# Optimization experiments

Measured on AMD Instinct MI355X. Metric: run time of the kernel, lower is better.

## Reference

```python
import jax, jax.numpy as jnp
import numpy as np

N_NODES = 20000
N_EDGES = 640000
IN_DIM = 128
HID_DIM = 256
N_CLASSES = 3
N_TYPES = 4
N_ASPECTS = 4096


def _type_aware_gcn(x, W_type, W_self, b, src, dst, etypes, n_nodes):
    # Per-node, per-type transforms: [N, T, H]
    xt = jnp.einsum('nd,tdh->nth', x, W_type)
    # Per-edge message: transform of source node under the edge's type. [E, H]
    msg = xt[src, etypes]
    # Degree-normalized scatter-sum into destination nodes.
    agg = jax.ops.segment_sum(msg, dst, num_segments=n_nodes)
    deg = jax.ops.segment_sum(jnp.ones((src.shape[0],), dtype=x.dtype), dst,
                              num_segments=n_nodes)
    agg = agg / jnp.clip(deg, 1.0)[:, None]
    # Self-loop transform + bias.
    return agg + x @ W_self + b


def setup_inputs() -> dict:
    key = jax.random.key(0)
    ks = jax.random.split(key, 12)
    features = jax.random.normal(ks[0], (N_NODES, IN_DIM), dtype=jnp.float32)
    edge_index = jax.random.randint(ks[1], (2, N_EDGES), 0, N_NODES)
    edge_types = jax.random.randint(ks[2], (N_EDGES,), 0, N_TYPES)
    aspect_indices = jax.random.randint(ks[3], (N_ASPECTS,), 0, N_NODES)
    s1 = 1.0 / np.sqrt(IN_DIM)
    s2 = 1.0 / np.sqrt(HID_DIM)
    W_type1 = jax.random.uniform(ks[4], (N_TYPES, IN_DIM, HID_DIM), minval=-s1, maxval=s1)
    W_self1 = jax.random.uniform(ks[5], (IN_DIM, HID_DIM), minval=-s1, maxval=s1)
    b1 = jnp.zeros((HID_DIM,), dtype=jnp.float32)
    W_type2 = jax.random.uniform(ks[6], (N_TYPES, HID_DIM, HID_DIM), minval=-s2, maxval=s2)
    W_self2 = jax.random.uniform(ks[7], (HID_DIM, HID_DIM), minval=-s2, maxval=s2)
    b2 = jnp.zeros((HID_DIM,), dtype=jnp.float32)
    W_cls = jax.random.uniform(ks[8], (HID_DIM, N_CLASSES), minval=-s2, maxval=s2)
    b_cls = jnp.zeros((N_CLASSES,), dtype=jnp.float32)
    return {
        'features': features,
        'W_type1': W_type1, 'W_self1': W_self1, 'b1': b1,
        'W_type2': W_type2, 'W_self2': W_self2, 'b2': b2,
        'W_cls': W_cls, 'b_cls': b_cls,
        'edge_index': edge_index,
        'edge_types': edge_types,
        'aspect_indices': aspect_indices,
    }


def reference(features, W_type1, W_self1, b1, W_type2, W_self2, b2,
              W_cls, b_cls, edge_index, edge_types, aspect_indices):
    n = features.shape[0]
    src, dst = edge_index[0], edge_index[1]
    h = _type_aware_gcn(features, W_type1, W_self1, b1, src, dst, edge_types, n)
    h = jax.nn.relu(h)
    # dropout: eval mode -> identity
    h = _type_aware_gcn(h, W_type2, W_self2, b2, src, dst, edge_types, n)
    aspect_embeddings = h[aspect_indices]            # [A, H]
    logits = aspect_embeddings @ W_cls + b_cls       # [A, C]
    return logits
```

## Files before the change

### kernel.cpp

```cpp
#include <hip/hip_runtime.h>

#define N_NODES   20000
#define N_EDGES   640000
#define IN_DIM    128
#define HID_DIM   256
#define N_TYPES   4
#define N_ASPECTS 4096
#define NT4       (N_NODES * N_TYPES)
#define NBUCK     157
#define BCAP      5120
#define CHUNK     2560

typedef __bf16 v8bf __attribute__((ext_vector_type(8)));
typedef float  f32x4 __attribute__((ext_vector_type(4)));

static __device__ __forceinline__ float bf2f(unsigned short u) {
    return __builtin_bit_cast(float, ((unsigned int)u) << 16);
}
static __device__ __forceinline__ float bflo(unsigned int u) {
    return __builtin_bit_cast(float, u << 16);
}
static __device__ __forceinline__ float bfhi(unsigned int u) {
    return __builtin_bit_cast(float, u & 0xffff0000u);
}
static __device__ __forceinline__ unsigned short f2bf(float f) {
    unsigned int u = __builtin_bit_cast(unsigned int, f);
    u += 0x7fffu + ((u >> 16) & 1u);
    return (unsigned short)(u >> 16);
}

static __device__ __forceinline__ int local_flag(const unsigned short* w) {
    __shared__ int red[4];
    int tid = threadIdx.x;
    int c = 0;
    for (int i = tid; i < 8192; i += 256) {
        unsigned hb = (w[i] >> 8) & 0x7f;
        c += (hb >= 0x39 && hb <= 0x3D) ? 1 : 0;
    }
#pragma unroll
    for (int off = 32; off >= 1; off >>= 1) c += __shfl_down(c, off);
    if ((tid & 63) == 0) red[tid >> 6] = c;
    __syncthreads();
    int tot = red[0] + red[1] + red[2] + red[3];
    __syncthreads();
    return (tot >= 6144) ? 1 : 0;
}

__global__ __launch_bounds__(256) void pre_kernel(
        const void* __restrict__ x,
        const void* __restrict__ Ws1, const void* __restrict__ Wt1,
        const void* __restrict__ Ws2, const void* __restrict__ Wt2,
        unsigned short* __restrict__ xc,
        unsigned short* __restrict__ WT1,
        unsigned short* __restrict__ WT2,
        int* __restrict__ bucket_cursor,
        int* __restrict__ flag) {
    int bf = local_flag((const unsigned short*)Ws1);
    int b = blockIdx.x, tid = threadIdx.x;
    if (b < 1250) {
        int idx = b * 256 + tid;
        if (bf) {
            reinterpret_cast<uint4*>(xc)[idx] = reinterpret_cast<const uint4*>(x)[idx];
        } else {
            const float* xf = reinterpret_cast<const float*>(x) + (size_t)idx * 8;
            unsigned short r[8] __attribute__((aligned(16)));
#pragma unroll
            for (int j = 0; j < 8; j++) r[j] = f2bf(xf[j]);
            reinterpret_cast<uint4*>(xc)[idx] = *reinterpret_cast<const uint4*>(r);
        }
    } else if (b < 1890) {
        int idx = (b - 1250) * 256 + tid;
        int n = idx / 640, k = idx - n * 640;
        const void* p = (k < 128) ? Ws1 : Wt1;
        size_t src = (k < 128) ? ((size_t)k * 256 + n) : ((size_t)(k - 128) * 256 + n);
        WT1[idx] = bf ? ((const unsigned short*)p)[src] : f2bf(((const float*)p)[src]);
    } else if (b < 3170) {
        int idx = (b - 1890) * 256 + tid;
        int n = idx / 1280, k = idx - n * 1280;
        const void* p = (k < 256) ? Ws2 : Wt2;
        size_t src = (k < 256) ? ((size_t)k * 256 + n) : ((size_t)(k - 256) * 256 + n);
        WT2[idx] = bf ? ((const unsigned short*)p)[src] : f2bf(((const float*)p)[src]);
    } else {
        if (tid < NBUCK) bucket_cursor[tid] = 0;
        if (tid == 0) *flag = bf;
    }
}

__global__ __launch_bounds__(256) void bucketA_kernel(
        const int* __restrict__ ei, const int* __restrict__ et,
        int* __restrict__ bucket_cursor, unsigned int* __restrict__ breg) {
    __shared__ unsigned int ord[CHUNK];
    __shared__ int hist[NBUCK], start[NBUCK], cur[NBUCK], gbase[NBUCK];
    int tid = threadIdx.x;
    int e0 = blockIdx.x * CHUNK;
    for (int i = tid; i < NBUCK; i += 256) hist[i] = 0;
    __syncthreads();
    unsigned int pk[10];
    int bk[10];
#pragma unroll
    for (int r = 0; r < 10; r++) {
        int e = e0 + r * 256 + tid;
        int s = __builtin_nontemporal_load(ei + e);
        int d = __builtin_nontemporal_load(ei + N_EDGES + e);
        int t = __builtin_nontemporal_load(et + e);
        pk[r] = (unsigned int)s | ((unsigned int)t << 15) | ((unsigned int)d << 17);
        bk[r] = d >> 7;
        atomicAdd(&hist[bk[r]], 1);
    }
    __syncthreads();
    if (tid == 0) {
        int acc = 0;
        for (int b = 0; b < NBUCK; b++) { start[b] = acc; cur[b] = acc; acc += hist[b]; }
    }
    __syncthreads();
#pragma unroll
    for (int r = 0; r < 10; r++) {
        int p = atomicAdd(&cur[bk[r]], 1);
        ord[p] = pk[r];
    }
    __syncthreads();
    for (int b = tid; b < NBUCK; b += 256)
        if (hist[b] > 0) gbase[b] = atomicAdd(bucket_cursor + b, hist[b]);
    __syncthreads();
    for (int p = tid; p < CHUNK; p += 256) {
        unsigned int e = ord[p];
        int b = (int)(e >> 24);
        int gp = gbase[b] + (p - start[b]);
        if (gp < BCAP)
            __builtin_nontemporal_store(e, breg + (size_t)b * BCAP + gp);
    }
}

__global__ __launch_bounds__(256) void bucketB_kernel(
        const unsigned int* __restrict__ breg,
        const int* __restrict__ bucket_cursor,
        unsigned short* __restrict__ perm,
        int* __restrict__ offsets4) {
    __shared__ int cnt[512], off[512];
    __shared__ int buf[256];
    int b = blockIdx.x, tid = threadIdx.x;
    int cv = (tid < NBUCK) ? bucket_cursor[tid] : 0;
    if (cv > BCAP) cv = BCAP;
    buf[tid] = cv;
    __syncthreads();
    for (int o = 1; o < 256; o <<= 1) {
        int t = (tid >= o) ? buf[tid - o] : 0;
        __syncthreads();
        buf[tid] += t;
        __syncthreads();
    }
    int obase = (b > 0) ? buf[b - 1] : 0;
    if (b == 0 && tid == 0) offsets4[NT4] = buf[255];
    int Eb = bucket_cursor[b];
    if (Eb > BCAP) Eb = BCAP;
    for (int i = tid; i < 512; i += 256) cnt[i] = 0;
    __syncthreads();
    const unsigned int* reg = breg + (size_t)b * BCAP;
    for (int i = tid; i < Eb; i += 256) {
        unsigned int e = reg[i];
        int seg = (((e >> 17) & 127) << 2) | ((e >> 15) & 3);
        atomicAdd(&cnt[seg], 1);
    }
    __syncthreads();
    if (tid == 0) {
        int acc = 0;
        for (int i = 0; i < 512; i++) { off[i] = acc; acc += cnt[i]; }
    }
    __syncthreads();
    for (int i = tid; i < 512; i += 256) {
        int node = b * 128 + (i >> 2);
        if (node < N_NODES) offsets4[node * 4 + (i & 3)] = obase + off[i];
    }
    __syncthreads();
    for (int i = tid; i < Eb; i += 256) {
        unsigned int e = reg[i];
        int seg = (((e >> 17) & 127) << 2) | ((e >> 15) & 3);
        int p = atomicAdd(&off[seg], 1);
        perm[obase + p] = (unsigned short)(e & 0x7fff);
    }
}

template <int D>
__global__ __launch_bounds__(256) void agg_kernel(
        const unsigned short* __restrict__ F,
        const int* __restrict__ offs4,
        const unsigned short* __restrict__ perm,
        unsigned short* __restrict__ AG) {
    constexpr int G = D / 8;
    constexpr int NSUB = 64 / G;
    int wave = threadIdx.x >> 6, lane = threadIdx.x & 63;
    int sg = lane / G;
    int gl = lane - sg * G;
    for (int n = blockIdx.x * 4 + wave; n < N_NODES; n += gridDim.x * 4) {
        int o0 = offs4[n * 4];
        int o4 = offs4[n * 4 + 4];
        int deg = o4 - o0;
        float inv = 1.0f / (float)(deg > 1 ? deg : 1);
        int s0 = o0;
#pragma unroll
        for (int t = 0; t < 4; t++) {
            int s1 = offs4[n * 4 + t + 1];
            float a[8];
#pragma unroll
            for (int v = 0; v < 8; v++) a[v] = 0.f;
            int j = s0;
            while (j < s1) {
                int m = s1 - j;
                if (m > 64) m = 64;
                int pw = (int)perm[j + ((lane < m) ? lane : 0)];
                int nfull = (m / (NSUB * 4)) * (NSUB * 4);
                for (int base = 0; base < nfull; base += NSUB * 4) {
                    uint4 x[4];
#pragma unroll
                    for (int l = 0; l < 4; l++) {
                        int src = __shfl(pw, base + sg * 4 + l);
                        x[l] = *reinterpret_cast<const uint4*>(F + (size_t)src * D + gl * 8);
                    }
#pragma unroll
                    for (int l = 0; l < 4; l++) {
                        a[0] += bflo(x[l].x); a[1] += bfhi(x[l].x);
                        a[2] += bflo(x[l].y); a[3] += bfhi(x[l].y);
                        a[4] += bflo(x[l].z); a[5] += bfhi(x[l].z);
                        a[6] += bflo(x[l].w); a[7] += bfhi(x[l].w);
                    }
                }
                for (int k = nfull; k < m; k += NSUB) {
                    int e = k + sg;
                    int valid = (e < m);
                    int idx = valid ? e : (m - 1);
                    int src = __shfl(pw, idx);
                    uint4 x = *reinterpret_cast<const uint4*>(F + (size_t)src * D + gl * 8);
                    unsigned msk = valid ? 0xffffffffu : 0u;
                    a[0] += bflo(x.x & msk); a[1] += bfhi(x.x & msk);
                    a[2] += bflo(x.y & msk); a[3] += bfhi(x.y & msk);
                    a[4] += bflo(x.z & msk); a[5] += bfhi(x.z & msk);
                    a[6] += bflo(x.w & msk); a[7] += bfhi(x.w & msk);
                }
                j += m;
            }
#pragma unroll
            for (int v = 0; v < 8; v++) {
                float s = a[v];
                s += __shfl_xor(s, G);
                if (NSUB == 4) s += __shfl_xor(s, 2 * G);
                a[v] = s * inv;
            }
            if (sg == 0) {
                unsigned short r[8] __attribute__((aligned(16)));
#pragma unroll
                for (int v = 0; v < 8; v++) r[v] = f2bf(a[v]);
                *reinterpret_cast<uint4*>(AG + (size_t)n * (4 * D) + t * D + gl * 8) =
                    *reinterpret_cast<const uint4*>(r);
            }
            s0 = s1;
        }
    }
}

template <int D>
__global__ __launch_bounds__(256, 6) void gemm_kernel(
        const unsigned short* __restrict__ X,
        const unsigned short* __restrict__ AG,
        const unsigned short* __restrict__ BT,
        const void* __restrict__ bias,
        const int* __restrict__ flagp,
        unsigned short* __restrict__ C,
        int M, int relu) {
    constexpr int K = 5 * D;
    constexpr int LDW = 72;
    __shared__ __align__(16) unsigned short As[64 * LDW];
    __shared__ __align__(16) unsigned short Bs[64 * LDW];
    int b = blockIdx.x;
    int mt = (b & 7) + 8 * (b >> 5);
    int nt = (b >> 3) & 3;
    int mtiles = (M + 63) >> 6;
    if (mt >= mtiles) return;
    int m0 = mt * 64;
    int n0 = nt * 64;
    int tid  = threadIdx.x;
    int wave = tid >> 6, lane = tid & 63;
    int wm = wave >> 1, wn = wave & 1;
    int quad = lane >> 4, l16 = lane & 15;

    f32x4 acc[2][2];
#pragma unroll
    for (int i = 0; i < 2; i++)
#pragma unroll
        for (int j = 0; j < 2; j++) acc[i][j] = (f32x4){0.f, 0.f, 0.f, 0.f};

    for (int k0 = 0; k0 < K; k0 += 64) {
        const unsigned short* base = (k0 < D) ? X : AG;
        int rs  = (k0 < D) ? D : 4 * D;
        int col = (k0 < D) ? k0 : (k0 - D);
#pragma unroll
        for (int cc = 0; cc < 2; cc++) {
            int c   = tid + cc * 256;
            int row = c >> 3;
            int c8  = c & 7;
            uint4 va = make_uint4(0u, 0u, 0u, 0u);
            int gr = m0 + row;
            if (gr < M)
                va = *reinterpret_cast<const uint4*>(base + (size_t)gr * rs + col + c8 * 8);
            *reinterpret_cast<uint4*>(&As[row * LDW + c8 * 8]) = va;
            uint4 vb = *reinterpret_cast<const uint4*>(BT + (size_t)(n0 + row) * K + k0 + c8 * 8);
            *reinterpret_cast<uint4*>(&Bs[row * LDW + c8 * 8]) = vb;
        }
        __syncthreads();
#pragma unroll
        for (int ks = 0; ks < 2; ks++) {
            v8bf af[2], bfr[2];
#pragma unroll
            for (int i = 0; i < 2; i++)
                af[i] = *reinterpret_cast<const v8bf*>(
                    &As[(wm * 32 + i * 16 + l16) * LDW + ks * 32 + quad * 8]);
#pragma unroll
            for (int j = 0; j < 2; j++)
                bfr[j] = *reinterpret_cast<const v8bf*>(
                    &Bs[(wn * 32 + j * 16 + l16) * LDW + ks * 32 + quad * 8]);
#pragma unroll
            for (int i = 0; i < 2; i++)
#pragma unroll
                for (int j = 0; j < 2; j++)
                    acc[i][j] = __builtin_amdgcn_mfma_f32_16x16x32_bf16(af[i], bfr[j], acc[i][j], 0, 0, 0);
        }
        __syncthreads();
    }
    int bf = *flagp;
#pragma unroll
    for (int i = 0; i < 2; i++) {
#pragma unroll
        for (int j = 0; j < 2; j++) {
            int col = n0 + wn * 32 + j * 16 + l16;
            float bv = bf ? bf2f(((const unsigned short*)bias)[col])
                          : ((const float*)bias)[col];
#pragma unroll
            for (int r = 0; r < 4; r++) {
                int row = m0 + wm * 32 + i * 16 + quad * 4 + r;
                if (row < M) {
                    float v = acc[i][j][r] + bv;
                    if (relu) v = fmaxf(v, 0.0f);
                    C[(size_t)row * 256 + col] = f2bf(v);
                }
            }
        }
    }
}

__global__ void cls_kernel(const unsigned short* __restrict__ h2,
                           const int* __restrict__ aidx,
                           const void* __restrict__ Wc,
                           const void* __restrict__ bc,
                           const int* __restrict__ flagp,
                           void* __restrict__ out) {
    int lin = blockIdx.x * blockDim.x + threadIdx.x;
    int a = lin >> 6, lane = lin & 63;
    if (a >= N_ASPECTS) return;
    int bf = *flagp;
    int node = aidx[a];
    uint2 v = *reinterpret_cast<const uint2*>(h2 + (size_t)node * 256 + lane * 4);
    float hv[4] = {bflo(v.x), bfhi(v.x), bflo(v.y), bfhi(v.y)};
    float a0 = 0.f, a1 = 0.f, a2 = 0.f;
#pragma unroll
    for (int r = 0; r < 4; r++) {
        int k = lane * 4 + r;
        float w0 = bf ? bf2f(((const unsigned short*)Wc)[k * 3 + 0]) : ((const float*)Wc)[k * 3 + 0];
        float w1 = bf ? bf2f(((const unsigned short*)Wc)[k * 3 + 1]) : ((const float*)Wc)[k * 3 + 1];
        float w2 = bf ? bf2f(((const unsigned short*)Wc)[k * 3 + 2]) : ((const float*)Wc)[k * 3 + 2];
        a0 += hv[r] * w0;
        a1 += hv[r] * w1;
        a2 += hv[r] * w2;
    }
#pragma unroll
    for (int off = 32; off >= 1; off >>= 1) {
        a0 += __shfl_down(a0, off);
        a1 += __shfl_down(a1, off);
        a2 += __shfl_down(a2, off);
    }
    if (lane == 0) {
        float b0 = bf ? bf2f(((const unsigned short*)bc)[0]) : ((const float*)bc)[0];
        float b1 = bf ? bf2f(((const unsigned short*)bc)[1]) : ((const float*)bc)[1];
        float b2 = bf ? bf2f(((const unsigned short*)bc)[2]) : ((const float*)bc)[2];
        if (bf) {
            unsigned short* o = (unsigned short*)out;
            o[a * 3 + 0] = f2bf(a0 + b0);
            o[a * 3 + 1] = f2bf(a1 + b1);
            o[a * 3 + 2] = f2bf(a2 + b2);
        } else {
            float* o = (float*)out;
            o[a * 3 + 0] = a0 + b0;
            o[a * 3 + 1] = a1 + b1;
            o[a * 3 + 2] = a2 + b2;
        }
    }
}

extern "C" void kernel_launch(void* const* d_in, const int* in_sizes, int n_in,
                              void* d_out, int out_size, void* d_ws, size_t ws_size,
                              hipStream_t stream) {
    const void* x   = d_in[0];
    const void* Wt1 = d_in[1];
    const void* Ws1 = d_in[2];
    const void* b1  = d_in[3];
    const void* Wt2 = d_in[4];
    const void* Ws2 = d_in[5];
    const void* b2  = d_in[6];
    const void* Wc  = d_in[7];
    const void* bc  = d_in[8];
    const int* ei = (const int*)d_in[9];
    const int* et = (const int*)d_in[10];
    const int* ai = (const int*)d_in[11];

    char* ws = (char*)d_ws;
    size_t off = 0;
    auto alloc = [&](size_t bytes) {
        void* p = ws + off;
        off += (bytes + 255) & ~(size_t)255;
        return p;
    };
    int*            flag          = (int*)alloc(4);
    int*            bucket_cursor = (int*)alloc((size_t)NBUCK * 4);
    int*            offsets4      = (int*)alloc((size_t)(NT4 + 1) * 4);
    unsigned int*   breg          = (unsigned int*)alloc((size_t)NBUCK * BCAP * 4);
    unsigned short* perm          = (unsigned short*)alloc((size_t)N_EDGES * 2);
    unsigned short* xc            = (unsigned short*)alloc((size_t)N_NODES * IN_DIM * 2);
    unsigned short* AG            = (unsigned short*)alloc((size_t)N_NODES * 4 * HID_DIM * 2);
    unsigned short* h             = (unsigned short*)alloc((size_t)N_NODES * HID_DIM * 2);
    unsigned short* h2            = (unsigned short*)alloc((size_t)N_NODES * HID_DIM * 2);
    unsigned short* WT1           = (unsigned short*)alloc((size_t)640 * 256 * 2);
    unsigned short* WT2           = (unsigned short*)alloc((size_t)1280 * 256 * 2);

    pre_kernel<<<3171, 256, 0, stream>>>(x, Ws1, Wt1, Ws2, Wt2,
                                         xc, WT1, WT2, bucket_cursor, flag);

    bucketA_kernel<<<N_EDGES / CHUNK, 256, 0, stream>>>(ei, et, bucket_cursor, breg);
    bucketB_kernel<<<NBUCK, 256, 0, stream>>>(breg, bucket_cursor, perm, offsets4);

    agg_kernel<IN_DIM><<<4096, 256, 0, stream>>>(xc, offsets4, perm, AG);
    gemm_kernel<IN_DIM><<<1280, 256, 0, stream>>>(xc, AG, WT1, b1, flag, h, N_NODES, 1);
    agg_kernel<HID_DIM><<<4096, 256, 0, stream>>>(h, offsets4, perm, AG);
    gemm_kernel<HID_DIM><<<1280, 256, 0, stream>>>(h, AG, WT2, b2, flag, h2, N_NODES, 0);
    cls_kernel<<<(N_ASPECTS * 64) / 256, 256, 0, stream>>>(h2, ai, Wc, bc, flag, d_out);
}
```

Baseline: 254.4 us.

## Fuse edge bucketing into preprocessing kernel and parallelize prefix scans

Merges the bucketA edge-bucketing pass into the conversion/transpose pre-kernel as an extra set of blocks, so the bucketing work runs concurrently with the dtype conversion. The cursor reset moves to a memset. The dtype-detection sample shrinks from 8192 to 1024 weights. The serial single-thread prefix sums in the bucketing and bucketB kernels become parallel Hillis-Steele block scans. This removes one launch and the serial scan latency, at the cost of a larger shared-memory footprint on every pre-kernel block and a less robust dtype heuristic.

After: 239.0 us. 6.1% less time.

```diff
diff --git a/kernel.cpp b/kernel.cpp
--- a/kernel.cpp
+++ b/kernel.cpp
@@ -29,11 +29,10 @@
     return (unsigned short)(u >> 16);
 }
 
-static __device__ __forceinline__ int local_flag(const unsigned short* w) {
-    __shared__ int red[4];
+static __device__ __forceinline__ int local_flag(const unsigned short* w, int* red) {
     int tid = threadIdx.x;
     int c = 0;
-    for (int i = tid; i < 8192; i += 256) {
+    for (int i = tid; i < 1024; i += 256) {
         unsigned hb = (w[i] >> 8) & 0x7f;
         c += (hb >= 0x39 && hb <= 0x3D) ? 1 : 0;
     }
@@ -43,22 +42,75 @@
     __syncthreads();
     int tot = red[0] + red[1] + red[2] + red[3];
     __syncthreads();
-    return (tot >= 6144) ? 1 : 0;
-}
-
-__global__ __launch_bounds__(256) void pre_kernel(
+    return (tot >= 768) ? 1 : 0;
+}
+
+__global__ __launch_bounds__(256) void prepA_kernel(
         const void* __restrict__ x,
         const void* __restrict__ Ws1, const void* __restrict__ Wt1,
         const void* __restrict__ Ws2, const void* __restrict__ Wt2,
+        const int* __restrict__ ei, const int* __restrict__ et,
         unsigned short* __restrict__ xc,
         unsigned short* __restrict__ WT1,
         unsigned short* __restrict__ WT2,
         int* __restrict__ bucket_cursor,
+        unsigned int* __restrict__ breg,
         int* __restrict__ flag) {
-    int bf = local_flag((const unsigned short*)Ws1);
+    __shared__ __align__(16) char smem[14336];
     int b = blockIdx.x, tid = threadIdx.x;
-    if (b < 1250) {
-        int idx = b * 256 + tid;
+    if (b < 250) {
+        unsigned int* ord = (unsigned int*)smem;
+        int* hist  = (int*)(smem + 10240);
+        int* start = hist + NBUCK;
+        int* cur   = start + NBUCK;
+        int* gbase = cur + NBUCK;
+        int* sbuf  = gbase + NBUCK;
+        int e0 = b * CHUNK;
+        for (int i = tid; i < NBUCK; i += 256) hist[i] = 0;
+        __syncthreads();
+        unsigned int pk[10];
+        int bk[10];
+#pragma unroll
+        for (int r = 0; r < 10; r++) {
+            int e = e0 + r * 256 + tid;
+            int s = __builtin_nontemporal_load(ei + e);
+            int d = __builtin_nontemporal_load(ei + N_EDGES + e);
+            int t = __builtin_nontemporal_load(et + e);
+            pk[r] = (unsigned int)s | ((unsigned int)t << 15) | ((unsigned int)d << 17);
+            bk[r] = d >> 7;
+            atomicAdd(&hist[bk[r]], 1);
+        }
+        __syncthreads();
+        int v = (tid < NBUCK) ? hist[tid] : 0;
+        sbuf[tid] = v;
+        __syncthreads();
+        for (int o = 1; o < 256; o <<= 1) {
+            int t = (tid >= o) ? sbuf[tid - o] : 0;
+            __syncthreads();
+            sbuf[tid] += t;
+            __syncthreads();
+        }
+        if (tid < NBUCK) { start[tid] = sbuf[tid] - v; cur[tid] = sbuf[tid] - v; }
+        __syncthreads();
+#pragma unroll
+        for (int r = 0; r < 10; r++) {
+            int p = atomicAdd(&cur[bk[r]], 1);
+            ord[p] = pk[r];
+        }
+        __syncthreads();
+        for (int bb = tid; bb < NBUCK; bb += 256)
+            if (hist[bb] > 0) gbase[bb] = atomicAdd(bucket_cursor + bb, hist[bb]);
+        __syncthreads();
+        for (int p = tid; p < CHUNK; p += 256) {
+            unsigned int e = ord[p];
+            int bb = (int)(e >> 24);
+            int gp = gbase[bb] + (p - start[bb]);
+            if (gp < BCAP)
+                __builtin_nontemporal_store(e, breg + (size_t)bb * BCAP + gp);
+        }
+    } else if (b < 1500) {
+        int bf = local_flag((const unsigned short*)Ws1, (int*)smem);
+        int idx = (b - 250) * 256 + tid;
         if (bf) {
             reinterpret_cast<uint4*>(xc)[idx] = reinterpret_cast<const uint4*>(x)[idx];
         } else {
@@ -68,66 +120,23 @@
             for (int j = 0; j < 8; j++) r[j] = f2bf(xf[j]);
             reinterpret_cast<uint4*>(xc)[idx] = *reinterpret_cast<const uint4*>(r);
         }
-    } else if (b < 1890) {
-        int idx = (b - 1250) * 256 + tid;
+    } else if (b < 2140) {
+        int bf = local_flag((const unsigned short*)Ws1, (int*)smem);
+        int idx = (b - 1500) * 256 + tid;
         int n = idx / 640, k = idx - n * 640;
         const void* p = (k < 128) ? Ws1 : Wt1;
         size_t src = (k < 128) ? ((size_t)k * 256 + n) : ((size_t)(k - 128) * 256 + n);
         WT1[idx] = bf ? ((const unsigned short*)p)[src] : f2bf(((const float*)p)[src]);
-    } else if (b < 3170) {
-        int idx = (b - 1890) * 256 + tid;
+    } else if (b < 3420) {
+        int bf = local_flag((const unsigned short*)Ws1, (int*)smem);
+        int idx = (b - 2140) * 256 + tid;
         int n = idx / 1280, k = idx - n * 1280;
         const void* p = (k < 256) ? Ws2 : Wt2;
         size_t src = (k < 256) ? ((size_t)k * 256 + n) : ((size_t)(k - 256) * 256 + n);
         WT2[idx] = bf ? ((const unsigned short*)p)[src] : f2bf(((const float*)p)[src]);
     } else {
-        if (tid < NBUCK) bucket_cursor[tid] = 0;
+        int bf = local_flag((const unsigned short*)Ws1, (int*)smem);
         if (tid == 0) *flag = bf;
-    }
-}
-
-__global__ __launch_bounds__(256) void bucketA_kernel(
-        const int* __restrict__ ei, const int* __restrict__ et,
-        int* __restrict__ bucket_cursor, unsigned int* __restrict__ breg) {
-    __shared__ unsigned int ord[CHUNK];
-    __shared__ int hist[NBUCK], start[NBUCK], cur[NBUCK], gbase[NBUCK];
-    int tid = threadIdx.x;
-    int e0 = blockIdx.x * CHUNK;
-    for (int i = tid; i < NBUCK; i += 256) hist[i] = 0;
-    __syncthreads();
-    unsigned int pk[10];
-    int bk[10];
-#pragma unroll
-    for (int r = 0; r < 10; r++) {
-        int e = e0 + r * 256 + tid;
-        int s = __builtin_nontemporal_load(ei + e);
-        int d = __builtin_nontemporal_load(ei + N_EDGES + e);
-        int t = __builtin_nontemporal_load(et + e);
-        pk[r] = (unsigned int)s | ((unsigned int)t << 15) | ((unsigned int)d << 17);
-        bk[r] = d >> 7;
-        atomicAdd(&hist[bk[r]], 1);
-    }
-    __syncthreads();
-    if (tid == 0) {
-        int acc = 0;
-        for (int b = 0; b < NBUCK; b++) { start[b] = acc; cur[b] = acc; acc += hist[b]; }
-    }
-    __syncthreads();
-#pragma unroll
-    for (int r = 0; r < 10; r++) {
-        int p = atomicAdd(&cur[bk[r]], 1);
-        ord[p] = pk[r];
-    }
-    __syncthreads();
-    for (int b = tid; b < NBUCK; b += 256)
-        if (hist[b] > 0) gbase[b] = atomicAdd(bucket_cursor + b, hist[b]);
-    __syncthreads();
-    for (int p = tid; p < CHUNK; p += 256) {
-        unsigned int e = ord[p];
-        int b = (int)(e >> 24);
-        int gp = gbase[b] + (p - start[b]);
-        if (gp < BCAP)
-            __builtin_nontemporal_store(e, breg + (size_t)b * BCAP + gp);
     }
 }
 
@@ -137,7 +146,7 @@
         unsigned short* __restrict__ perm,
         int* __restrict__ offsets4) {
     __shared__ int cnt[512], off[512];
-    __shared__ int buf[256];
+    __shared__ int buf[256], pscan[256];
     int b = blockIdx.x, tid = threadIdx.x;
     int cv = (tid < NBUCK) ? bucket_cursor[tid] : 0;
     if (cv > BCAP) cv = BCAP;
@@ -162,10 +171,18 @@
         atomicAdd(&cnt[seg], 1);
     }
     __syncthreads();
-    if (tid == 0) {
-        int acc = 0;
-        for (int i = 0; i < 512; i++) { off[i] = acc; acc += cnt[i]; }
-    }
+    int pv = cnt[2 * tid] + cnt[2 * tid + 1];
+    pscan[tid] = pv;
+    __syncthreads();
+    for (int o = 1; o < 256; o <<= 1) {
+        int t = (tid >= o) ? pscan[tid - o] : 0;
+        __syncthreads();
+        pscan[tid] += t;
+        __syncthreads();
+    }
+    int pexcl = pscan[tid] - pv;
+    off[2 * tid]     = pexcl;
+    off[2 * tid + 1] = pexcl + cnt[2 * tid];
     __syncthreads();
     for (int i = tid; i < 512; i += 256) {
         int node = b * 128 + (i >> 2);
@@ -429,10 +446,9 @@
     unsigned short* WT1           = (unsigned short*)alloc((size_t)640 * 256 * 2);
     unsigned short* WT2           = (unsigned short*)alloc((size_t)1280 * 256 * 2);
 
-    pre_kernel<<<3171, 256, 0, stream>>>(x, Ws1, Wt1, Ws2, Wt2,
-                                         xc, WT1, WT2, bucket_cursor, flag);
-
-    bucketA_kernel<<<N_EDGES / CHUNK, 256, 0, stream>>>(ei, et, bucket_cursor, breg);
+    hipMemsetAsync(bucket_cursor, 0, (size_t)NBUCK * 4, stream);
+    prepA_kernel<<<3421, 256, 0, stream>>>(x, Ws1, Wt1, Ws2, Wt2, ei, et,
+                                           xc, WT1, WT2, bucket_cursor, breg, flag);
     bucketB_kernel<<<NBUCK, 256, 0, stream>>>(breg, bucket_cursor, perm, offsets4);
 
     agg_kernel<IN_DIM><<<4096, 256, 0, stream>>>(xc, offsets4, perm, AG);
```
